# Kernel optimization log

Hardware: AMD Instinct MI355X
Metric: run time of the kernel (lower is better)

Reference implementation:

```python
import jax, jax.numpy as jnp
import numpy as np

S = 4096
F = 512  # in_features, head_num == 1 so per-head dim == F


def setup_inputs() -> dict:
    key = jax.random.key(0)
    ks = jax.random.split(key, 11)
    std = 0.02
    inp = {
        "q": jax.random.normal(ks[0], (1, S, F), jnp.float32),
        "k": jax.random.normal(ks[1], (1, S, F), jnp.float32),
        "v": jax.random.normal(ks[2], (1, S, F), jnp.float32),
        "Wq": jax.random.normal(ks[3], (F, F), jnp.float32) * std,
        "bq": jax.random.normal(ks[4], (F,), jnp.float32) * std,
        "Wk": jax.random.normal(ks[5], (F, F), jnp.float32) * std,
        "bk": jax.random.normal(ks[6], (F,), jnp.float32) * std,
        "Wv": jax.random.normal(ks[7], (F, F), jnp.float32) * std,
        "bv": jax.random.normal(ks[8], (F,), jnp.float32) * std,
        "Wo": jax.random.normal(ks[9], (F, F), jnp.float32) * std,
        "bo": jax.random.normal(ks[10], (F,), jnp.float32) * std,
    }
    return inp


def reference(q, k, v, Wq, bq, Wk, bk, Wv, bv, Wo, bo):
    dk = Wq.shape[0]  # head_num == 1 -> per-head dim equals in_features
    # q_k, q_v: projections of q WITHOUT activation (as in original forward)
    q_k = q @ Wk.T + bk            # (1, S, F)
    q_v = q @ Wv.T + bv            # (1, S, F)
    # activated projections (F.relu)
    qq = jax.nn.relu(q @ Wq.T + bq)[0]  # (S, F)
    kk = jax.nn.relu(k @ Wk.T + bk)[0]  # (S, F)
    vv = jax.nn.relu(v @ Wv.T + bv)[0]  # (S, F)
    # diagonal of qq @ q_k^T, computed without materializing the SxS matrix
    q_att = jnp.sum(qq * q_k[0], axis=-1, keepdims=True)  # (S, 1)
    scores = jnp.einsum('sd,td->st', qq, kk)               # (S, S)
    scores = jnp.concatenate([scores, q_att], axis=-1)     # (S, S+1)
    scores = scores / np.sqrt(dk + 1).astype(np.float32)
    attn = jax.nn.softmax(scores, axis=-1)                 # (S, S+1)
    res = attn[:, :-1] @ vv                                # (S, F)
    res = q_v[0] * q_att + res                             # elementwise fusion
    y = res[None]                                          # (1, S, F)
    y = jax.nn.relu(y @ Wo.T + bo)
    return y
```

## Files before the change

kernel.cpp:

```cpp
#include <hip/hip_runtime.h>
#include <math.h>

#define S_LEN 4096
#define F_DIM 512
#define PSPLIT 8
#define FIXED_M 4.0f
#define SCALE_QK 0.04415108f

typedef __attribute__((ext_vector_type(8))) short bf16x8;
typedef __attribute__((ext_vector_type(4))) float f32x4;

__device__ __forceinline__ unsigned short f2bf(float x) {
    union { float f; unsigned u; } v; v.f = x;
    unsigned r = v.u + 0x7fffu + ((v.u >> 16) & 1u);
    return (unsigned short)(r >> 16);
}
__device__ __forceinline__ float bf2f(unsigned short b) {
    union { unsigned u; float f; } v; v.u = ((unsigned)b) << 16;
    return v.f;
}
__device__ __forceinline__ void load_lds16(const void* g, void* l) {
    __builtin_amdgcn_global_load_lds(
        (const __attribute__((address_space(1))) unsigned int*)g,
        (__attribute__((address_space(3))) unsigned int*)l, 16, 0, 0);
}

struct CastArgs {
    const float* src[7];
    unsigned short* dst[7];
    int n4[7];
};
__global__ void cast_all(CastArgs a) {
    int r = blockIdx.y;
    int i = blockIdx.x * blockDim.x + threadIdx.x;
    if (i >= a.n4[r]) return;
    float4 v = ((const float4*)a.src[r])[i];
    ushort4 o;
    o.x = f2bf(v.x); o.y = f2bf(v.y); o.z = f2bf(v.z); o.w = f2bf(v.w);
    ((ushort4*)a.dst[r])[i] = o;
}

__global__ void transpose_bf16(const unsigned short* __restrict__ src,
                               unsigned short* __restrict__ dst) {
    __shared__ __align__(16) unsigned short tile[64][72];
    const int s0 = blockIdx.x * 64, f0 = blockIdx.y * 64;
    const int tid = threadIdx.x;
#pragma unroll
    for (int it = 0; it < 2; ++it) {
        int u = it * 256 + tid;
        int r = u >> 3, c = (u & 7) * 8;
        *(uint4*)&tile[r][c] = *(const uint4*)(src + (size_t)(s0 + r) * F_DIM + f0 + c);
    }
    __syncthreads();
#pragma unroll
    for (int it = 0; it < 2; ++it) {
        int u = it * 256 + tid;
        int fl = u >> 3, sc = (u & 7) * 8;
        unsigned short tmp[8];
#pragma unroll
        for (int i = 0; i < 8; ++i) tmp[i] = tile[sc + i][fl];
        *(uint4*)(dst + (size_t)(f0 + fl) * S_LEN + s0 + sc) = *(uint4*)tmp;
    }
}

struct GemmDesc {
    const unsigned short* X;
    const unsigned short* W;
    const float* bias;
    unsigned short* out_bf;
    float* out_f32;
    int relu;
};
struct GemmArgs { GemmDesc d[5]; };

#define FRAGA(qm) { _Pragma("unroll") for (int mt = 0; mt < 4; ++mt) { \
    const int ro = (aw + (qm) * 64 + mt * 16) * 64 + rbase; \
    af[mt][0] = *(const bf16x8*)&Ac[ro + q0]; \
    af[mt][1] = *(const bf16x8*)&Ac[ro + q1]; } }

#define FRAGB(qn) { _Pragma("unroll") for (int nt = 0; nt < 2; ++nt) { \
    const int ro = (bw + (qn) * 32 + nt * 16) * 64 + rbase; \
    bf[nt][0] = *(const bf16x8*)&Bc[ro + q0]; \
    bf[nt][1] = *(const bf16x8*)&Bc[ro + q1]; } }

#define MMQ(qm, qn) { __builtin_amdgcn_s_setprio(1); \
    _Pragma("unroll") for (int kh = 0; kh < 2; ++kh) \
    _Pragma("unroll") for (int mt = 0; mt < 4; ++mt) \
    _Pragma("unroll") for (int nt = 0; nt < 2; ++nt) \
      acc[(qm) * 4 + mt][(qn) * 2 + nt] = __builtin_amdgcn_mfma_f32_16x16x32_bf16( \
          af[mt][kh], bf[nt][kh], acc[(qm) * 4 + mt][(qn) * 2 + nt], 0, 0, 0); \
    __builtin_amdgcn_s_setprio(0); }

__device__ __forceinline__ void kloop256(const unsigned short* __restrict__ A, int lda,
                                         const unsigned short* __restrict__ B, int ldb,
                                         int m0, int n0, int kbase,
                                         unsigned short* smem, f32x4 acc[8][4]) {
    const int tid = threadIdx.x;
    const int w = tid >> 6, l = tid & 63;
    const int ln = l & 15, quad = l >> 4, lnx = l & 7;
    const int wm = w >> 2, wn = w & 3;
    const int srow = l >> 3;
    const int scol = (lnx ^ srow) * 8;
    const int rbase = ln * 64;
    const int q0 = (quad ^ lnx) * 8;
    const int q1 = ((4 + quad) ^ lnx) * 8;
    unsigned short* As = smem;
    unsigned short* Bs = smem + 32768;
    const unsigned short* Asrc = A + (size_t)(m0 + srow) * lda + kbase + scol;
    const unsigned short* Bsrc = B + (size_t)(n0 + srow) * ldb + kbase + scol;

    auto stageA = [&](int dd, int ktn) {
#pragma unroll
        for (int j = 0; j < 4; ++j) {
            int chunk = w * 4 + j;
            load_lds16(Asrc + (size_t)(chunk * 8) * lda + ktn * 64,
                       &As[dd * 16384 + chunk * 512]);
        }
    };
    auto stageB = [&](int dd, int ktn) {
#pragma unroll
        for (int j = 0; j < 4; ++j) {
            int chunk = w * 4 + j;
            load_lds16(Bsrc + (size_t)(chunk * 8) * ldb + ktn * 64,
                       &Bs[dd * 16384 + chunk * 512]);
        }
    };

    stageA(0, 0); stageB(0, 0);
    asm volatile("s_waitcnt vmcnt(0)" ::: "memory");
    __builtin_amdgcn_s_barrier();

#pragma unroll
    for (int kt = 0; kt < 8; ++kt) {
        const int d = kt & 1;
        const unsigned short* Ac = &As[d * 16384];
        const unsigned short* Bc = &Bs[d * 16384];
        const int aw = wm * 128, bw = wn * 64;
        bf16x8 af[4][2], bf[2][2];

        FRAGA(0); FRAGB(0);
        if (kt < 7) stageA(d ^ 1, kt + 1);
        __builtin_amdgcn_s_barrier();
        MMQ(0, 0);
        __builtin_amdgcn_s_barrier();

        FRAGB(1);
        if (kt < 7) stageB(d ^ 1, kt + 1);
        __builtin_amdgcn_s_barrier();
        MMQ(0, 1);
        __builtin_amdgcn_s_barrier();

        FRAGA(1);
        __builtin_amdgcn_s_barrier();
        MMQ(1, 1);
        __builtin_amdgcn_s_barrier();

        FRAGB(0);
        __builtin_amdgcn_s_barrier();
        MMQ(1, 0);
        asm volatile("s_waitcnt vmcnt(0)" ::: "memory");
        __builtin_amdgcn_s_barrier();
    }
}

__launch_bounds__(512, 2)
__global__ void gemm_proj2(GemmArgs args) {
    extern __shared__ unsigned short smem[];
    const GemmDesc d = args.d[blockIdx.y >> 1];
    const int n0 = (blockIdx.y & 1) * 256;
    const int m0 = blockIdx.x * 256;
    f32x4 acc[8][4];
    f32x4 z = {0.f, 0.f, 0.f, 0.f};
#pragma unroll
    for (int i = 0; i < 8; ++i)
#pragma unroll
        for (int j = 0; j < 4; ++j) acc[i][j] = z;

    kloop256(d.X, F_DIM, d.W, F_DIM, m0, n0, 0, smem, acc);

    const int tid = threadIdx.x;
    const int w = tid >> 6, l = tid & 63, quad = l >> 4, ln = l & 15;
    const int wm = w >> 2, wn = w & 3;
#pragma unroll
    for (int mi = 0; mi < 8; ++mi)
#pragma unroll
        for (int ni = 0; ni < 4; ++ni)
#pragma unroll
            for (int r = 0; r < 4; ++r) {
                int row = m0 + wm * 128 + mi * 16 + quad * 4 + r;
                int col = n0 + wn * 64 + ni * 16 + ln;
                float vv = acc[mi][ni][r] + d.bias[col];
                if (d.relu) vv = fmaxf(vv, 0.f);
                if (d.out_bf)  d.out_bf[(size_t)row * F_DIM + col] = f2bf(vv);
                if (d.out_f32) d.out_f32[(size_t)row * F_DIM + col] = vv;
            }
}

__launch_bounds__(512, 2)
__global__ void gemm_exp2(const unsigned short* __restrict__ X,
                          const unsigned short* __restrict__ W,
                          unsigned short* __restrict__ P,
                          float* __restrict__ lpart) {
    extern __shared__ unsigned short smem[];
    const int m0 = blockIdx.x * 256, n0 = blockIdx.y * 256;
    f32x4 acc[8][4];
    f32x4 z = {0.f, 0.f, 0.f, 0.f};
#pragma unroll
    for (int i = 0; i < 8; ++i)
#pragma unroll
        for (int j = 0; j < 4; ++j) acc[i][j] = z;

    kloop256(X, F_DIM, W, F_DIM, m0, n0, 0, smem, acc);

    const int tid = threadIdx.x;
    const int w = tid >> 6, l = tid & 63, quad = l >> 4, ln = l & 15;
    const int wm = w >> 2, wn = w & 3;
#pragma unroll
    for (int mi = 0; mi < 8; ++mi)
#pragma unroll
        for (int r = 0; r < 4; ++r) {
            int row = m0 + wm * 128 + mi * 16 + quad * 4 + r;
            float rs = 0.f;
#pragma unroll
            for (int ni = 0; ni < 4; ++ni) {
                int col = n0 + wn * 64 + ni * 16 + ln;
                float p = __expf(acc[mi][ni][r] * SCALE_QK - FIXED_M);
                P[(size_t)row * S_LEN + col] = f2bf(p);
                rs += p;
            }
            rs += __shfl_xor(rs, 1);
            rs += __shfl_xor(rs, 2);
            rs += __shfl_xor(rs, 4);
            rs += __shfl_xor(rs, 8);
            if (ln == 0) lpart[(size_t)row * 64 + blockIdx.y * 4 + wn] = rs;
        }
}

__launch_bounds__(512, 2)
__global__ void gemm_pv2(const unsigned short* __restrict__ P,
                         const unsigned short* __restrict__ vt,
                         unsigned short* __restrict__ O_p) {
    extern __shared__ unsigned short smem[];
    const int nb = blockIdx.y & 1, split = blockIdx.y >> 1;
    const int m0 = blockIdx.x * 256, n0 = nb * 256;
    f32x4 acc[8][4];
    f32x4 z = {0.f, 0.f, 0.f, 0.f};
#pragma unroll
    for (int i = 0; i < 8; ++i)
#pragma unroll
        for (int j = 0; j < 4; ++j) acc[i][j] = z;

    kloop256(P, S_LEN, vt, S_LEN, m0, n0, split * (S_LEN / PSPLIT), smem, acc);

    unsigned short* Op = O_p + (size_t)split * S_LEN * F_DIM;
    const int tid = threadIdx.x;
    const int w = tid >> 6, l = tid & 63, quad = l >> 4, ln = l & 15;
    const int wm = w >> 2, wn = w & 3;
#pragma unroll
    for (int mi = 0; mi < 8; ++mi)
#pragma unroll
        for (int ni = 0; ni < 4; ++ni)
#pragma unroll
            for (int r = 0; r < 4; ++r) {
                int row = m0 + wm * 128 + mi * 16 + quad * 4 + r;
                int col = n0 + wn * 64 + ni * 16 + ln;
                Op[(size_t)row * F_DIM + col] = f2bf(acc[mi][ni][r]);
            }
}

#define GEMM_KLOOP(XPTR, LDX, WPTR, LDW, KBEG, KEND)                                  \
    for (int k0 = (KBEG); k0 < (KEND); k0 += 64) {                                    \
        __syncthreads();                                                              \
        _Pragma("unroll")                                                             \
        for (int i = 0; i < 2; ++i) {                                                 \
            int c = w * 2 + i;                                                        \
            _Pragma("unroll")                                                         \
            for (int kh = 0; kh < 2; ++kh) {                                          \
                load_lds16((XPTR) + (size_t)(m0 + c * 16 + ln) * (LDX) + k0 + kh * 32 + quad * 8, \
                           &As[(c * 2 + kh) * 512]);                                  \
                load_lds16((WPTR) + (size_t)(n0 + c * 16 + ln) * (LDW) + k0 + kh * 32 + quad * 8, \
                           &Bs[(c * 2 + kh) * 512]);                                  \
            }                                                                         \
        }                                                                             \
        __syncthreads();                                                              \
        _Pragma("unroll")                                                             \
        for (int kh = 0; kh < 2; ++kh) {                                              \
            bf16x8 af2[4], bfr2[4];                                                   \
            _Pragma("unroll")                                                         \
            for (int mt = 0; mt < 4; ++mt)                                            \
                af2[mt] = *(const bf16x8*)&As[((wr * 4 + mt) * 2 + kh) * 512 + l * 8]; \
            _Pragma("unroll")                                                         \
            for (int nt = 0; nt < 4; ++nt)                                            \
                bfr2[nt] = *(const bf16x8*)&Bs[((wc * 4 + nt) * 2 + kh) * 512 + l * 8]; \
            _Pragma("unroll")                                                         \
            for (int mt = 0; mt < 4; ++mt)                                            \
                _Pragma("unroll")                                                     \
                for (int nt = 0; nt < 4; ++nt)                                        \
                    acc[mt][nt] = __builtin_amdgcn_mfma_f32_16x16x32_bf16(            \
                        af2[mt], bfr2[nt], acc[mt][nt], 0, 0, 0);                     \
        }                                                                             \
    }

__launch_bounds__(256, 2)
__global__ void gemm_final(const unsigned short* __restrict__ X,
                           const unsigned short* __restrict__ W,
                           float* __restrict__ Fp) {
    __shared__ __align__(16) unsigned short As[16 * 512];
    __shared__ __align__(16) unsigned short Bs[16 * 512];
    const int nb = blockIdx.y & 3;
    const int kseg = blockIdx.y >> 2;
    const int n0 = nb * 128;
    const int m0 = blockIdx.x * 128;
    const int tid = threadIdx.x;
    const int w = tid >> 6, l = tid & 63, quad = l >> 4, ln = l & 15;
    const int wr = w >> 1, wc = w & 1;

    f32x4 acc[4][4];
    f32x4 zero4 = {0.f, 0.f, 0.f, 0.f};
#pragma unroll
    for (int i = 0; i < 4; ++i)
#pragma unroll
        for (int j = 0; j < 4; ++j) acc[i][j] = zero4;

    GEMM_KLOOP(X, F_DIM, W, F_DIM, kseg * 256, kseg * 256 + 256)

    float* Op = Fp + (size_t)kseg * S_LEN * F_DIM;
#pragma unroll
    for (int mt = 0; mt < 4; ++mt)
#pragma unroll
        for (int nt = 0; nt < 4; ++nt)
#pragma unroll
            for (int r = 0; r < 4; ++r) {
                int row = m0 + wr * 64 + mt * 16 + quad * 4 + r;
                int col = n0 + wc * 64 + nt * 16 + ln;
                Op[(size_t)row * F_DIM + col] = acc[mt][nt][r];
            }
}

__global__ void reduce_final(const float* __restrict__ Fp,
                             const float* __restrict__ bias,
                             float* __restrict__ out) {
    int i = blockIdx.x * blockDim.x + threadIdx.x;
    int col4 = (i & (F_DIM / 4 - 1)) * 4;
    float4 a = ((const float4*)Fp)[i];
    float4 b = ((const float4*)(Fp + (size_t)S_LEN * F_DIM))[i];
    float4 bi = *(const float4*)(bias + col4);
    float4 o;
    o.x = fmaxf(a.x + b.x + bi.x, 0.f);
    o.y = fmaxf(a.y + b.y + bi.y, 0.f);
    o.z = fmaxf(a.z + b.z + bi.z, 0.f);
    o.w = fmaxf(a.w + b.w + bi.w, 0.f);
    ((float4*)out)[i] = o;
}

__global__ void combine_kernel(const unsigned short* __restrict__ O_p,
                               const float* __restrict__ lpart,
                               const unsigned short* __restrict__ qq,
                               const unsigned short* __restrict__ qk,
                               const unsigned short* __restrict__ qv,
                               unsigned short* __restrict__ res_bf) {
    int row = blockIdx.x;
    int t = threadIdx.x;
    int wv = t >> 6, l = t & 63;
    __shared__ float ws[4];

    ushort4 a = *(const ushort4*)(qq + (size_t)row * F_DIM + t * 4);
    ushort4 b = *(const ushort4*)(qk + (size_t)row * F_DIM + t * 4);
    float dotp = bf2f(a.x) * bf2f(b.x) + bf2f(a.y) * bf2f(b.y) +
                 bf2f(a.z) * bf2f(b.z) + bf2f(a.w) * bf2f(b.w);
    float lp = (t < 64) ? lpart[(size_t)row * 64 + t] : 0.f;
#pragma unroll
    for (int off = 32; off >= 1; off >>= 1) {
        dotp += __shfl_xor(dotp, off);
        lp += __shfl_xor(lp, off);
    }
    if (l == 0) { ws[wv] = dotp; ws[2 + wv] = lp; }
    __syncthreads();
    float qa = ws[0] + ws[1];
    float denom = __expf(qa * SCALE_QK - FIXED_M) + ws[2] + ws[3];
    float inv = 1.f / denom;

    float4 s = {0.f, 0.f, 0.f, 0.f};
#pragma unroll
    for (int i = 0; i < PSPLIT; ++i) {
        ushort4 o = *(const ushort4*)(O_p + ((size_t)i * S_LEN + row) * F_DIM + t * 4);
        s.x += bf2f(o.x); s.y += bf2f(o.y); s.z += bf2f(o.z); s.w += bf2f(o.w);
    }
    ushort4 qvv = *(const ushort4*)(qv + (size_t)row * F_DIM + t * 4);
    ushort4 o;
    o.x = f2bf(bf2f(qvv.x) * qa + s.x * inv);
    o.y = f2bf(bf2f(qvv.y) * qa + s.y * inv);
    o.z = f2bf(bf2f(qvv.z) * qa + s.z * inv);
    o.w = f2bf(bf2f(qvv.w) * qa + s.w * inv);
    *(ushort4*)(res_bf + (size_t)row * F_DIM + t * 4) = o;
}

extern "C" void kernel_launch(void* const* d_in, const int* in_sizes, int n_in,
                              void* d_out, int out_size, void* d_ws, size_t ws_size,
                              hipStream_t stream) {
    const float* q  = (const float*)d_in[0];
    const float* k  = (const float*)d_in[1];
    const float* v  = (const float*)d_in[2];
    const float* Wq = (const float*)d_in[3];
    const float* bq = (const float*)d_in[4];
    const float* Wk = (const float*)d_in[5];
    const float* bk = (const float*)d_in[6];
    const float* Wv = (const float*)d_in[7];
    const float* bv = (const float*)d_in[8];
    const float* Wo = (const float*)d_in[9];
    const float* bo = (const float*)d_in[10];
    float* out = (float*)d_out;

    char* p = (char*)d_ws;
    auto alloc = [&](size_t bytes) -> char* {
        char* r = p; p += (bytes + 255) & ~(size_t)255; return r;
    };
    const size_t SF = (size_t)S_LEN * F_DIM;
    unsigned short* q_bf  = (unsigned short*)alloc(SF * 2);
    unsigned short* k_bf  = (unsigned short*)alloc(SF * 2);
    unsigned short* v_bf  = (unsigned short*)alloc(SF * 2);
    unsigned short* qq_bf = (unsigned short*)alloc(SF * 2);
    unsigned short* kk_bf = (unsigned short*)alloc(SF * 2);
    unsigned short* vv_bf = (unsigned short*)alloc(SF * 2);
    unsigned short* vt_bf = (unsigned short*)alloc(SF * 2);
    unsigned short* qk_bf = (unsigned short*)alloc(SF * 2);
    unsigned short* qv_bf = (unsigned short*)alloc(SF * 2);
    unsigned short* res_bf = (unsigned short*)alloc(SF * 2);
    unsigned short* wq_bf = (unsigned short*)alloc((size_t)F_DIM * F_DIM * 2);
    unsigned short* wk_bf = (unsigned short*)alloc((size_t)F_DIM * F_DIM * 2);
    unsigned short* wv_bf = (unsigned short*)alloc((size_t)F_DIM * F_DIM * 2);
    unsigned short* wo_bf = (unsigned short*)alloc((size_t)F_DIM * F_DIM * 2);
    unsigned short* P_bf  = (unsigned short*)alloc((size_t)S_LEN * S_LEN * 2);
    float* lpart = (float*)alloc((size_t)S_LEN * 64 * 4);
    unsigned short* O_p = (unsigned short*)alloc((size_t)PSPLIT * SF * 2);
    float* Fp = (float*)alloc((size_t)2 * SF * 4);

    static int attr_done = 0;
    if (!attr_done) {
        hipFuncSetAttribute((const void*)gemm_proj2,
                            hipFuncAttributeMaxDynamicSharedMemorySize, 131072);
        hipFuncSetAttribute((const void*)gemm_exp2,
                            hipFuncAttributeMaxDynamicSharedMemorySize, 131072);
        hipFuncSetAttribute((const void*)gemm_pv2,
                            hipFuncAttributeMaxDynamicSharedMemorySize, 131072);
        attr_done = 1;
    }

    CastArgs ca;
    ca.src[0] = q;  ca.dst[0] = q_bf;  ca.n4[0] = (int)(SF / 4);
    ca.src[1] = k;  ca.dst[1] = k_bf;  ca.n4[1] = (int)(SF / 4);
    ca.src[2] = v;  ca.dst[2] = v_bf;  ca.n4[2] = (int)(SF / 4);
    ca.src[3] = Wq; ca.dst[3] = wq_bf; ca.n4[3] = F_DIM * F_DIM / 4;
    ca.src[4] = Wk; ca.dst[4] = wk_bf; ca.n4[4] = F_DIM * F_DIM / 4;
    ca.src[5] = Wv; ca.dst[5] = wv_bf; ca.n4[5] = F_DIM * F_DIM / 4;
    ca.src[6] = Wo; ca.dst[6] = wo_bf; ca.n4[6] = F_DIM * F_DIM / 4;
    cast_all<<<dim3((unsigned)(SF / 4 / 256), 7), 256, 0, stream>>>(ca);

    GemmArgs ga;
    ga.d[0] = { q_bf, wq_bf, bq, qq_bf, nullptr, 1 };
    ga.d[1] = { k_bf, wk_bf, bk, kk_bf, nullptr, 1 };
    ga.d[2] = { v_bf, wv_bf, bv, vv_bf, nullptr, 1 };
    ga.d[3] = { q_bf, wk_bf, bk, qk_bf, nullptr, 0 };
    ga.d[4] = { q_bf, wv_bf, bv, qv_bf, nullptr, 0 };
    gemm_proj2<<<dim3(S_LEN / 256, 10), 512, 131072, stream>>>(ga);

    transpose_bf16<<<dim3(S_LEN / 64, F_DIM / 64), 256, 0, stream>>>(vv_bf, vt_bf);

    gemm_exp2<<<dim3(S_LEN / 256, S_LEN / 256), 512, 131072, stream>>>(qq_bf, kk_bf, P_bf, lpart);

    gemm_pv2<<<dim3(S_LEN / 256, 2 * PSPLIT), 512, 131072, stream>>>(P_bf, vt_bf, O_p);

    combine_kernel<<<S_LEN, 128, 0, stream>>>(O_p, lpart, qq_bf, qk_bf, qv_bf, res_bf);

    gemm_final<<<dim3(S_LEN / 128, 8), 256, 0, stream>>>(res_bf, wo_bf, Fp);
    reduce_final<<<(unsigned)(SF / 4 / 256), 256, 0, stream>>>(Fp, bo, out);
}
```

Baseline: 199.7 us.

## Switch main GEMMs to 32x32x16 MFMA and drop split-K final GEMM

After: 210.9 us. 5.6% more time.

```diff
diff --git a/kernel.cpp b/kernel.cpp
--- a/kernel.cpp
+++ b/kernel.cpp
@@ -9,6 +9,7 @@
 
 typedef __attribute__((ext_vector_type(8))) short bf16x8;
 typedef __attribute__((ext_vector_type(4))) float f32x4;
+typedef __attribute__((ext_vector_type(16))) float f32x16;
 
 __device__ __forceinline__ unsigned short f2bf(float x) {
     union { float f; unsigned u; } v; v.f = x;
@@ -73,37 +74,32 @@
 };
 struct GemmArgs { GemmDesc d[5]; };
 
-#define FRAGA(qm) { _Pragma("unroll") for (int mt = 0; mt < 4; ++mt) { \
-    const int ro = (aw + (qm) * 64 + mt * 16) * 64 + rbase; \
-    af[mt][0] = *(const bf16x8*)&Ac[ro + q0]; \
-    af[mt][1] = *(const bf16x8*)&Ac[ro + q1]; } }
-
-#define FRAGB(qn) { _Pragma("unroll") for (int nt = 0; nt < 2; ++nt) { \
-    const int ro = (bw + (qn) * 32 + nt * 16) * 64 + rbase; \
-    bf[nt][0] = *(const bf16x8*)&Bc[ro + q0]; \
-    bf[nt][1] = *(const bf16x8*)&Bc[ro + q1]; } }
-
-#define MMQ(qm, qn) { __builtin_amdgcn_s_setprio(1); \
-    _Pragma("unroll") for (int kh = 0; kh < 2; ++kh) \
-    _Pragma("unroll") for (int mt = 0; mt < 4; ++mt) \
-    _Pragma("unroll") for (int nt = 0; nt < 2; ++nt) \
-      acc[(qm) * 4 + mt][(qn) * 2 + nt] = __builtin_amdgcn_mfma_f32_16x16x32_bf16( \
-          af[mt][kh], bf[nt][kh], acc[(qm) * 4 + mt][(qn) * 2 + nt], 0, 0, 0); \
+#define FRAGA32(qm) { _Pragma("unroll") for (int fr = 0; fr < 2; ++fr) \
+    _Pragma("unroll") for (int ks = 0; ks < 4; ++ks) { \
+      const int rw = aw + (qm) * 64 + fr * 32 + l31; \
+      af[fr][ks] = *(const bf16x8*)&Ac[rw * 64 + ((ks * 2 + lhi) ^ lnx) * 8]; } }
+
+#define FRAGB32(qn) { _Pragma("unroll") for (int ks = 0; ks < 4; ++ks) { \
+      const int rw = bw + (qn) * 32 + l31; \
+      bfr[ks] = *(const bf16x8*)&Bc[rw * 64 + ((ks * 2 + lhi) ^ lnx) * 8]; } }
+
+#define MMQ32(qm, qn) { __builtin_amdgcn_s_setprio(1); \
+    _Pragma("unroll") for (int ks = 0; ks < 4; ++ks) \
+    _Pragma("unroll") for (int fr = 0; fr < 2; ++fr) \
+      acc[(qm) * 2 + fr][qn] = __builtin_amdgcn_mfma_f32_32x32x16_bf16( \
+          af[fr][ks], bfr[ks], acc[(qm) * 2 + fr][qn], 0, 0, 0); \
     __builtin_amdgcn_s_setprio(0); }
 
 __device__ __forceinline__ void kloop256(const unsigned short* __restrict__ A, int lda,
                                          const unsigned short* __restrict__ B, int ldb,
                                          int m0, int n0, int kbase,
-                                         unsigned short* smem, f32x4 acc[8][4]) {
+                                         unsigned short* smem, f32x16 acc[4][2]) {
     const int tid = threadIdx.x;
     const int w = tid >> 6, l = tid & 63;
-    const int ln = l & 15, quad = l >> 4, lnx = l & 7;
+    const int l31 = l & 31, lhi = l >> 5, lnx = l & 7;
     const int wm = w >> 2, wn = w & 3;
     const int srow = l >> 3;
     const int scol = (lnx ^ srow) * 8;
-    const int rbase = ln * 64;
-    const int q0 = (quad ^ lnx) * 8;
-    const int q1 = ((4 + quad) ^ lnx) * 8;
     unsigned short* As = smem;
     unsigned short* Bs = smem + 32768;
     const unsigned short* Asrc = A + (size_t)(m0 + srow) * lda + kbase + scol;
@@ -136,32 +132,33 @@
         const unsigned short* Ac = &As[d * 16384];
         const unsigned short* Bc = &Bs[d * 16384];
         const int aw = wm * 128, bw = wn * 64;
-        bf16x8 af[4][2], bf[2][2];
-
-        FRAGA(0); FRAGB(0);
-        if (kt < 7) stageA(d ^ 1, kt + 1);
-        __builtin_amdgcn_s_barrier();
-        MMQ(0, 0);
-        __builtin_amdgcn_s_barrier();
-
-        FRAGB(1);
-        if (kt < 7) stageB(d ^ 1, kt + 1);
-        __builtin_amdgcn_s_barrier();
-        MMQ(0, 1);
-        __builtin_amdgcn_s_barrier();
-
-        FRAGA(1);
-        __builtin_amdgcn_s_barrier();
-        MMQ(1, 1);
-        __builtin_amdgcn_s_barrier();
-
-        FRAGB(0);
-        __builtin_amdgcn_s_barrier();
-        MMQ(1, 0);
+        bf16x8 af[2][4], bfr[4];
+
+        FRAGA32(0); FRAGB32(0);
+        if (kt < 7) { stageA(d ^ 1, kt + 1); stageB(d ^ 1, kt + 1); }
+        __builtin_amdgcn_s_barrier();
+        MMQ32(0, 0);
+        __builtin_amdgcn_s_barrier();
+
+        FRAGB32(1);
+        __builtin_amdgcn_s_barrier();
+        MMQ32(0, 1);
+        __builtin_amdgcn_s_barrier();
+
+        FRAGA32(1);
+        __builtin_amdgcn_s_barrier();
+        MMQ32(1, 1);
+        __builtin_amdgcn_s_barrier();
+
+        FRAGB32(0);
+        __builtin_amdgcn_s_barrier();
+        MMQ32(1, 0);
         asm volatile("s_waitcnt vmcnt(0)" ::: "memory");
         __builtin_amdgcn_s_barrier();
     }
 }
+
+#define EPI_ROW(base, fa, r) ((base) + (fa) * 32 + ((r) & 3) + 8 * ((r) >> 2) + 4 * lhi)
 
 __launch_bounds__(512, 2)
 __global__ void gemm_proj2(GemmArgs args) {
@@ -169,27 +166,30 @@
     const GemmDesc d = args.d[blockIdx.y >> 1];
     const int n0 = (blockIdx.y & 1) * 256;
     const int m0 = blockIdx.x * 256;
-    f32x4 acc[8][4];
-    f32x4 z = {0.f, 0.f, 0.f, 0.f};
-#pragma unroll
-    for (int i = 0; i < 8; ++i)
-#pragma unroll
-        for (int j = 0; j < 4; ++j) acc[i][j] = z;
+    f32x16 acc[4][2];
+#pragma unroll
+    for (int i = 0; i < 4; ++i)
+#pragma unroll
+        for (int j = 0; j < 2; ++j)
+#pragma unroll
+            for (int e = 0; e < 16; ++e) acc[i][j][e] = 0.f;
 
     kloop256(d.X, F_DIM, d.W, F_DIM, m0, n0, 0, smem, acc);
 
     const int tid = threadIdx.x;
-    const int w = tid >> 6, l = tid & 63, quad = l >> 4, ln = l & 15;
+    const int w = tid >> 6, l = tid & 63, l31 = l & 31, lhi = l >> 5;
     const int wm = w >> 2, wn = w & 3;
-#pragma unroll
-    for (int mi = 0; mi < 8; ++mi)
-#pragma unroll
-        for (int ni = 0; ni < 4; ++ni)
-#pragma unroll
-            for (int r = 0; r < 4; ++r) {
-                int row = m0 + wm * 128 + mi * 16 + quad * 4 + r;
-                int col = n0 + wn * 64 + ni * 16 + ln;
-                float vv = acc[mi][ni][r] + d.bias[col];
+    const int rbase = m0 + wm * 128;
+    const int cbase = n0 + wn * 64;
+#pragma unroll
+    for (int fa = 0; fa < 4; ++fa)
+#pragma unroll
+        for (int fc = 0; fc < 2; ++fc)
+#pragma unroll
+            for (int r = 0; r < 16; ++r) {
+                int row = EPI_ROW(rbase, fa, r);
+                int col = cbase + fc * 32 + l31;
+                float vv = acc[fa][fc][r] + d.bias[col];
                 if (d.relu) vv = fmaxf(vv, 0.f);
                 if (d.out_bf)  d.out_bf[(size_t)row * F_DIM + col] = f2bf(vv);
                 if (d.out_f32) d.out_f32[(size_t)row * F_DIM + col] = vv;
@@ -203,36 +203,37 @@
                           float* __restrict__ lpart) {
     extern __shared__ unsigned short smem[];
     const int m0 = blockIdx.x * 256, n0 = blockIdx.y * 256;
-    f32x4 acc[8][4];
-    f32x4 z = {0.f, 0.f, 0.f, 0.f};
-#pragma unroll
-    for (int i = 0; i < 8; ++i)
-#pragma unroll
-        for (int j = 0; j < 4; ++j) acc[i][j] = z;
+    f32x16 acc[4][2];
+#pragma unroll
+    for (int i = 0; i < 4; ++i)
+#pragma unroll
+        for (int j = 0; j < 2; ++j)
+#pragma unroll
+            for (int e = 0; e < 16; ++e) acc[i][j][e] = 0.f;
 
     kloop256(X, F_DIM, W, F_DIM, m0, n0, 0, smem, acc);
 
     const int tid = threadIdx.x;
-    const int w = tid >> 6, l = tid & 63, quad = l >> 4, ln = l & 15;
+    const int w = tid >> 6, l = tid & 63, l31 = l & 31, lhi = l >> 5;
     const int wm = w >> 2, wn = w & 3;
-#pragma unroll
-    for (int mi = 0; mi < 8; ++mi)
-#pragma unroll
-        for (int r = 0; r < 4; ++r) {
-            int row = m0 + wm * 128 + mi * 16 + quad * 4 + r;
-            float rs = 0.f;
-#pragma unroll
-            for (int ni = 0; ni < 4; ++ni) {
-                int col = n0 + wn * 64 + ni * 16 + ln;
-                float p = __expf(acc[mi][ni][r] * SCALE_QK - FIXED_M);
-                P[(size_t)row * S_LEN + col] = f2bf(p);
-                rs += p;
-            }
+    const int rbase = m0 + wm * 128;
+    const int cbase = n0 + wn * 64;
+#pragma unroll
+    for (int fa = 0; fa < 4; ++fa)
+#pragma unroll
+        for (int r = 0; r < 16; ++r) {
+            int row = EPI_ROW(rbase, fa, r);
+            float p0 = __expf(acc[fa][0][r] * SCALE_QK - FIXED_M);
+            float p1 = __expf(acc[fa][1][r] * SCALE_QK - FIXED_M);
+            P[(size_t)row * S_LEN + cbase + l31] = f2bf(p0);
+            P[(size_t)row * S_LEN + cbase + 32 + l31] = f2bf(p1);
+            float rs = p0 + p1;
             rs += __shfl_xor(rs, 1);
             rs += __shfl_xor(rs, 2);
             rs += __shfl_xor(rs, 4);
             rs += __shfl_xor(rs, 8);
-            if (ln == 0) lpart[(size_t)row * 64 + blockIdx.y * 4 + wn] = rs;
+            rs += __shfl_xor(rs, 16);
+            if (l31 == 0) lpart[(size_t)row * 64 + blockIdx.y * 4 + wn] = rs;
         }
 }
 
@@ -243,28 +244,31 @@
     extern __shared__ unsigned short smem[];
     const int nb = blockIdx.y & 1, split = blockIdx.y >> 1;
     const int m0 = blockIdx.x * 256, n0 = nb * 256;
-    f32x4 acc[8][4];
-    f32x4 z = {0.f, 0.f, 0.f, 0.f};
-#pragma unroll
-    for (int i = 0; i < 8; ++i)
-#pragma unroll
-        for (int j = 0; j < 4; ++j) acc[i][j] = z;
+    f32x16 acc[4][2];
+#pragma unroll
+    for (int i = 0; i < 4; ++i)
+#pragma unroll
+        for (int j = 0; j < 2; ++j)
+#pragma unroll
+            for (int e = 0; e < 16; ++e) acc[i][j][e] = 0.f;
 
     kloop256(P, S_LEN, vt, S_LEN, m0, n0, split * (S_LEN / PSPLIT), smem, acc);
 
     unsigned short* Op = O_p + (size_t)split * S_LEN * F_DIM;
     const int tid = threadIdx.x;
-    const int w = tid >> 6, l = tid & 63, quad = l >> 4, ln = l & 15;
+    const int w = tid >> 6, l = tid & 63, l31 = l & 31, lhi = l >> 5;
     const int wm = w >> 2, wn = w & 3;
-#pragma unroll
-    for (int mi = 0; mi < 8; ++mi)
-#pragma unroll
-        for (int ni = 0; ni < 4; ++ni)
-#pragma unroll
-            for (int r = 0; r < 4; ++r) {
-                int row = m0 + wm * 128 + mi * 16 + quad * 4 + r;
-                int col = n0 + wn * 64 + ni * 16 + ln;
-                Op[(size_t)row * F_DIM + col] = f2bf(acc[mi][ni][r]);
+    const int rbase = m0 + wm * 128;
+    const int cbase = n0 + wn * 64;
+#pragma unroll
+    for (int fa = 0; fa < 4; ++fa)
+#pragma unroll
+        for (int fc = 0; fc < 2; ++fc)
+#pragma unroll
+            for (int r = 0; r < 16; ++r) {
+                int row = EPI_ROW(rbase, fa, r);
+                int col = cbase + fc * 32 + l31;
+                Op[(size_t)row * F_DIM + col] = f2bf(acc[fa][fc][r]);
             }
 }
 
@@ -304,12 +308,11 @@
 __launch_bounds__(256, 2)
 __global__ void gemm_final(const unsigned short* __restrict__ X,
                            const unsigned short* __restrict__ W,
-                           float* __restrict__ Fp) {
+                           const float* __restrict__ bias,
+                           float* __restrict__ out) {
     __shared__ __align__(16) unsigned short As[16 * 512];
     __shared__ __align__(16) unsigned short Bs[16 * 512];
-    const int nb = blockIdx.y & 3;
-    const int kseg = blockIdx.y >> 2;
-    const int n0 = nb * 128;
+    const int n0 = blockIdx.y * 128;
     const int m0 = blockIdx.x * 128;
     const int tid = threadIdx.x;
     const int w = tid >> 6, l = tid & 63, quad = l >> 4, ln = l & 15;
@@ -322,9 +325,8 @@
 #pragma unroll
         for (int j = 0; j < 4; ++j) acc[i][j] = zero4;
 
-    GEMM_KLOOP(X, F_DIM, W, F_DIM, kseg * 256, kseg * 256 + 256)
-
-    float* Op = Fp + (size_t)kseg * S_LEN * F_DIM;
+    GEMM_KLOOP(X, F_DIM, W, F_DIM, 0, F_DIM)
+
 #pragma unroll
     for (int mt = 0; mt < 4; ++mt)
 #pragma unroll
@@ -333,24 +335,9 @@
             for (int r = 0; r < 4; ++r) {
                 int row = m0 + wr * 64 + mt * 16 + quad * 4 + r;
                 int col = n0 + wc * 64 + nt * 16 + ln;
-                Op[(size_t)row * F_DIM + col] = acc[mt][nt][r];
+                out[(size_t)row * F_DIM + col] =
+                    fmaxf(acc[mt][nt][r] + bias[col], 0.f);
             }
-}
-
-__global__ void reduce_final(const float* __restrict__ Fp,
-                             const float* __restrict__ bias,
-                             float* __restrict__ out) {
-    int i = blockIdx.x * blockDim.x + threadIdx.x;
-    int col4 = (i & (F_DIM / 4 - 1)) * 4;
-    float4 a = ((const float4*)Fp)[i];
-    float4 b = ((const float4*)(Fp + (size_t)S_LEN * F_DIM))[i];
-    float4 bi = *(const float4*)(bias + col4);
-    float4 o;
-    o.x = fmaxf(a.x + b.x + bi.x, 0.f);
-    o.y = fmaxf(a.y + b.y + bi.y, 0.f);
-    o.z = fmaxf(a.z + b.z + bi.z, 0.f);
-    o.w = fmaxf(a.w + b.w + bi.w, 0.f);
-    ((float4*)out)[i] = o;
 }
 
 __global__ void combine_kernel(const unsigned short* __restrict__ O_p,
@@ -433,7 +420,6 @@
     unsigned short* P_bf  = (unsigned short*)alloc((size_t)S_LEN * S_LEN * 2);
     float* lpart = (float*)alloc((size_t)S_LEN * 64 * 4);
     unsigned short* O_p = (unsigned short*)alloc((size_t)PSPLIT * SF * 2);
-    float* Fp = (float*)alloc((size_t)2 * SF * 4);
 
     static int attr_done = 0;
     if (!attr_done) {
@@ -472,6 +458,5 @@
 
     combine_kernel<<<S_LEN, 128, 0, stream>>>(O_p, lpart, qq_bf, qk_bf, qv_bf, res_bf);
 
-    gemm_final<<<dim3(S_LEN / 128, 8), 256, 0, stream>>>(res_bf, wo_bf, Fp);
-    reduce_final<<<(unsigned)(SF / 4 / 256), 256, 0, stream>>>(Fp, bo, out);
-}
+    gemm_final<<<dim3(S_LEN / 128, 4), 256, 0, stream>>>(res_bf, wo_bf, bo, out);
+}
```
